# Performance work log

Hardware: AMD Instinct MI355X
Metric: run time of the kernel (lower is better)

## Reference

```python
import jax, jax.numpy as jnp
import numpy as np

SAMPLING_RATIO = 1.0


def gcn_conv(x, src, dst, ew, W, b):
    """PyG GCNConv: h = D^-1/2 (A+I) D^-1/2 (xW) + b, edges weighted by ew.
    Masked edges (ew=0) contribute neither messages nor degree, exactly
    matching running the conv on the subset edge_index."""
    n = x.shape[0]
    h = x @ W                                              # [N, out]
    deg = jax.ops.segment_sum(ew, dst, num_segments=n) + 1.0  # +1 for self-loop
    dinv = jax.lax.rsqrt(deg)                              # deg >= 1, safe
    norm = dinv[src] * dinv[dst] * ew                      # [E]
    agg = jax.ops.segment_sum(h[src] * norm[:, None], dst, num_segments=n)
    return agg + h * (dinv * dinv)[:, None] + b            # self-loop term + bias


def setup_inputs() -> dict:
    key = jax.random.key(0)
    ks = jax.random.split(key, 8)
    N, E, F_IN, HID, OUT = 50000, 800000, 128, 128, 64
    x = jax.random.normal(ks[0], (N, F_IN), dtype=jnp.float32)
    edge_index = jax.random.randint(ks[1], (2, E), 0, N, dtype=jnp.int32)
    edge_rand = jax.random.uniform(ks[2], (E,), dtype=jnp.float32)
    s0 = 1.0 / np.sqrt(F_IN)
    s1 = 1.0 / np.sqrt(HID)
    w0 = jax.random.normal(ks[3], (F_IN, HID), dtype=jnp.float32) * s0
    b0 = jnp.zeros((HID,), dtype=jnp.float32)
    w1 = jax.random.normal(ks[4], (HID, HID), dtype=jnp.float32) * s1
    b1 = jnp.zeros((HID,), dtype=jnp.float32)
    w2 = jax.random.normal(ks[5], (HID, OUT), dtype=jnp.float32) * s1
    b2 = jnp.zeros((OUT,), dtype=jnp.float32)
    return {"x": x, "edge_index": edge_index, "edge_rand": edge_rand,
            "w0": w0, "b0": b0, "w1": w1, "b1": b1, "w2": w2, "b2": b2}


def reference(x, edge_index, edge_rand, w0, b0, w1, b1, w2, b2):
    src, dst = edge_index[0], edge_index[1]
    ones = jnp.ones(src.shape, dtype=x.dtype)
    # first pass over full graph -> tmp_z
    z = jax.nn.relu(gcn_conv(x, src, dst, ones, w0, b0))
    z = jax.nn.relu(gcn_conv(z, src, dst, ones, w1, b1))
    tmp_z = gcn_conv(z, src, dst, ones, w2, b2)
    # edge sampling: gather-dot-sigmoid-threshold (detached mask)
    edge_logit = jnp.sum(tmp_z[src] * tmp_z[dst], axis=-1)
    edge_weight = jax.nn.sigmoid(edge_logit)
    mask = jax.lax.stop_gradient(
        (edge_weight > SAMPLING_RATIO * edge_rand).astype(x.dtype))
    # second pass: sampled edges for hidden layers, full edges for last layer
    h = jax.nn.relu(gcn_conv(x, src, dst, mask, w0, b0))
    h = jax.nn.relu(gcn_conv(h, src, dst, mask, w1, b1))
    out = gcn_conv(h, src, dst, ones, w2, b2)
    return out
```

## Files before the change

kernel.cpp:

```cpp
#include <hip/hip_runtime.h>


typedef __attribute__((ext_vector_type(8))) short bf16x8;
typedef __attribute__((ext_vector_type(4))) float f32x4;

__device__ inline unsigned bfpair(float lo, float hi) {
    unsigned a = __float_as_uint(lo), b = __float_as_uint(hi);
    a = (a + 0x7FFFu + ((a >> 16) & 1u)) >> 16;
    b = (b + 0x7FFFu + ((b >> 16) & 1u)) & 0xFFFF0000u;
    return a | b;
}
__device__ inline unsigned short bf1(float v) {
    unsigned u = __float_as_uint(v);
    return (unsigned short)((u + 0x7FFFu + ((u >> 16) & 1u)) >> 16);
}
__device__ inline void unpack2(unsigned u, float& f0, float& f1) {
    f0 = __uint_as_float(u << 16);
    f1 = __uint_as_float(u & 0xFFFF0000u);
}

__global__ void k_scan1(const int* __restrict__ in, int* __restrict__ out,
                        int* __restrict__ bsums, int N) {
    __shared__ int tmp[256];
    int i = blockIdx.x * 256 + threadIdx.x;
    int v = (i < N) ? in[i] : 0;
    tmp[threadIdx.x] = v;
    __syncthreads();
    for (int off = 1; off < 256; off <<= 1) {
        int t = (threadIdx.x >= off) ? tmp[threadIdx.x - off] : 0;
        __syncthreads();
        tmp[threadIdx.x] += t;
        __syncthreads();
    }
    if (i < N) out[i] = tmp[threadIdx.x] - v;
    if (threadIdx.x == 255) bsums[blockIdx.x] = tmp[255];
}

__global__ void k_scan2(int* __restrict__ bsums, int nb) {
    __shared__ int tmp[256];
    int v = (threadIdx.x < nb) ? bsums[threadIdx.x] : 0;
    tmp[threadIdx.x] = v;
    __syncthreads();
    for (int off = 1; off < 256; off <<= 1) {
        int t = (threadIdx.x >= off) ? tmp[threadIdx.x - off] : 0;
        __syncthreads();
        tmp[threadIdx.x] += t;
        __syncthreads();
    }
    if (threadIdx.x < nb) bsums[threadIdx.x] = tmp[threadIdx.x] - v;
}

__global__ void k_scan3(int* __restrict__ out, const int* __restrict__ bsums, int N, int E) {
    int i = blockIdx.x * 256 + threadIdx.x;
    if (i < N) out[i] += bsums[blockIdx.x];
    if (i == 0) out[N] = E;
}

__global__ __launch_bounds__(256) void k_bcount(const int* __restrict__ dst,
                                                int* __restrict__ cnt, int E, int chunk) {
    __shared__ int h[1024];
    for (int i = threadIdx.x; i < 1024; i += 256) h[i] = 0;
    __syncthreads();
    int beg = blockIdx.x * chunk, end = min(E, beg + chunk);
    for (int e = beg + threadIdx.x; e < end; e += 256)
        atomicAdd(&h[dst[e] >> 6], 1);
    __syncthreads();
    for (int b = threadIdx.x; b < 1024; b += 256)
        cnt[b * 64 + blockIdx.x] = h[b];
}

__global__ __launch_bounds__(256) void k_bscatter(const int* __restrict__ src,
                                                  const int* __restrict__ dst,
                                                  const float* __restrict__ er,
                                                  const int* __restrict__ sbase,
                                                  int2* __restrict__ stg, int E, int chunk) {
    __shared__ int cur[1024];
    for (int i = threadIdx.x; i < 1024; i += 256) cur[i] = 0;
    __syncthreads();
    int beg = blockIdx.x * chunk, end = min(E, beg + chunk);
    for (int e = beg + threadIdx.x; e < end; e += 256) {
        int d = dst[e];
        int b = d >> 6;
        int loc = atomicAdd(&cur[b], 1);
        int pos = sbase[b * 64 + blockIdx.x] + loc;
        stg[pos] = make_int2(src[e] | ((d & 63) << 16), (int)__float_as_uint(er[e]));
    }
}

__global__ __launch_bounds__(256) void k_bindeg(const int2* __restrict__ stg,
                                                const int* __restrict__ sbase,
                                                int* __restrict__ indeg, int N) {
    __shared__ int cnt[64];
    if (threadIdx.x < 64) cnt[threadIdx.x] = 0;
    __syncthreads();
    int b = blockIdx.x;
    int beg = sbase[b * 64], end = sbase[(b + 1) * 64];
    for (int i = beg + threadIdx.x; i < end; i += 256)
        atomicAdd(&cnt[(stg[i].x >> 16) & 63], 1);
    __syncthreads();
    if (threadIdx.x < 64) {
        int node = b * 64 + threadIdx.x;
        if (node < N) indeg[node] = cnt[threadIdx.x];
    }
}

__global__ __launch_bounds__(256) void k_bfill(const int2* __restrict__ stg,
                                               const int* __restrict__ sbase,
                                               const int* __restrict__ csr_off,
                                               const float* __restrict__ dinvF,
                                               int2* __restrict__ csr_se,
                                               float* __restrict__ coefF, int N) {
    __shared__ int cur[64];
    int b = blockIdx.x;
    if (threadIdx.x < 64) {
        int node = b * 64 + threadIdx.x;
        cur[threadIdx.x] = (node < N) ? csr_off[node] : 0;
    }
    __syncthreads();
    int beg = sbase[b * 64], end = sbase[(b + 1) * 64];
    for (int i = beg + threadIdx.x; i < end; i += 256) {
        int2 se = stg[i];
        int s = se.x & 0xFFFF;
        int j = (se.x >> 16) & 63;
        int pos = atomicAdd(&cur[j], 1);
        csr_se[pos] = make_int2(s, se.y);
        coefF[pos] = dinvF[s];
    }
}

__global__ void k_dinv(const int* __restrict__ deg, float* __restrict__ dinv, int N) {
    int i = blockIdx.x * blockDim.x + threadIdx.x;
    if (i < N) dinv[i] = 1.0f / sqrtf((float)deg[i] + 1.0f);
}

__global__ void k_coef_mask(const int2* __restrict__ csr_se, const float* __restrict__ dinv,
                            const float* __restrict__ survive, float* __restrict__ coef, int E) {
    int i = blockIdx.x * blockDim.x + threadIdx.x;
    if (i < E) coef[i] = dinv[csr_se[i].x] * survive[i];
}

__global__ __launch_bounds__(128) void k_surv(const float* __restrict__ tz,
                                              const int* __restrict__ csr_off,
                                              const int2* __restrict__ csr_se,
                                              float* __restrict__ survive,
                                              int* __restrict__ degm, int N) {
    const int v = blockIdx.x;
    const int l = threadIdx.x & 15;
    const int s = threadIdx.x >> 4;
    const int e0 = csr_off[v];
    const int e1 = csr_off[v + 1];
    const float4 tv = *(const float4*)&tz[(size_t)v * 64 + l * 4];
    int cnt = 0;
    for (int i = e0 + s; i < e1; i += 8) {
        int2 se = csr_se[i];
        const float4 a = *(const float4*)&tz[(size_t)se.x * 64 + l * 4];
        float p = a.x * tv.x + a.y * tv.y + a.z * tv.z + a.w * tv.w;
        p += __shfl_xor(p, 1, 16);
        p += __shfl_xor(p, 2, 16);
        p += __shfl_xor(p, 4, 16);
        p += __shfl_xor(p, 8, 16);
        float sg = 1.0f / (1.0f + expf(-p));
        float m = (sg > __uint_as_float((unsigned)se.y)) ? 1.0f : 0.0f;
        if (l == 0) {
            survive[i] = m;
            cnt += (m != 0.0f) ? 1 : 0;
        }
    }
    __shared__ int sc[8];
    if (l == 0) sc[s] = cnt;
    __syncthreads();
    if (threadIdx.x == 0) {
        int t = 0;
#pragma unroll
        for (int k = 0; k < 8; k++) t += sc[k];
        degm[v] = t;
    }
}

__global__ void k_packw3(const float* __restrict__ W, unsigned short* __restrict__ Wp,
                         int OUTC, int total) {
    int idx = blockIdx.x * 256 + threadIdx.x;
    if (idx >= total) return;
    int l = idx & 63;
    int tk = idx >> 6;
    int kb = tk & 3;
    int ct = tk >> 2;
    size_t PL = (size_t)(OUTC / 16) * 4 * 64 * 8;
    unsigned short v0[8], v1[8], v2[8];
#pragma unroll
    for (int i = 0; i < 8; i++) {
        float wv = W[(kb * 32 + ((l >> 4) * 8) + i) * OUTC + ct * 16 + (l & 15)];
        unsigned short h0 = bf1(wv);
        float f0 = __uint_as_float((unsigned)h0 << 16);
        float r1 = wv - f0;
        unsigned short h1 = bf1(r1);
        float f1 = __uint_as_float((unsigned)h1 << 16);
        unsigned short h2 = bf1(r1 - f1);
        v0[i] = h0; v1[i] = h1; v2[i] = h2;
    }
    auto st = [](unsigned short* dst, unsigned short* v) {
        uint4 u;
        u.x = v[0] | ((unsigned)v[1] << 16);
        u.y = v[2] | ((unsigned)v[3] << 16);
        u.z = v[4] | ((unsigned)v[5] << 16);
        u.w = v[6] | ((unsigned)v[7] << 16);
        *(uint4*)dst = u;
    };
    st(&Wp[(size_t)idx * 8], v0);
    st(&Wp[PL + (size_t)idx * 8], v1);
    st(&Wp[2 * PL + (size_t)idx * 8], v2);
}

template <int OUTC, bool WB16>
__global__ __launch_bounds__(256) void k_gemm_split(const float* __restrict__ A,
                                                    const unsigned short* __restrict__ Wp,
                                                    float* __restrict__ Cout,
                                                    unsigned short* __restrict__ Cb, int N) {
    constexpr int CT = OUTC / 16;
    constexpr int PL = CT * 4 * 64 * 8;
    constexpr int LDW = OUTC + 4;
    __shared__ float eps[64 * LDW];
    const int w = threadIdx.x >> 6;
    const int l = threadIdx.x & 63;
    int row = blockIdx.x * 64 + w * 16 + (l & 15);
    int rowc = (row < N) ? row : (N - 1);

    bf16x8 a0[4], a1[4], a2[4];
#pragma unroll
    for (int kb = 0; kb < 4; kb++) {
        const float* pa = &A[(size_t)rowc * 128 + kb * 32 + ((l >> 4) * 8)];
        float4 x0 = *(const float4*)pa;
        float4 x1 = *(const float4*)(pa + 4);
        float xa[8] = {x0.x, x0.y, x0.z, x0.w, x1.x, x1.y, x1.z, x1.w};
#pragma unroll
        for (int i = 0; i < 8; i++) {
            unsigned short h0 = bf1(xa[i]);
            float f0 = __uint_as_float((unsigned)h0 << 16);
            float r1 = xa[i] - f0;
            unsigned short h1 = bf1(r1);
            float f1 = __uint_as_float((unsigned)h1 << 16);
            unsigned short h2 = bf1(r1 - f1);
            a0[kb][i] = (short)h0;
            a1[kb][i] = (short)h1;
            a2[kb][i] = (short)h2;
        }
    }
#pragma unroll
    for (int ct = 0; ct < CT; ct++) {
        f32x4 accA = {0.f, 0.f, 0.f, 0.f};
        f32x4 accB = {0.f, 0.f, 0.f, 0.f};
#pragma unroll
        for (int kb = 0; kb < 4; kb++) {
            const size_t bo = ((size_t)(ct * 4 + kb) * 64 + l) * 8;
            bf16x8 b0 = *(const bf16x8*)&Wp[bo];
            bf16x8 b1 = *(const bf16x8*)&Wp[PL + bo];
            bf16x8 b2 = *(const bf16x8*)&Wp[2 * PL + bo];
            accA = __builtin_amdgcn_mfma_f32_16x16x32_bf16(a0[kb], b0, accA, 0, 0, 0);
            accB = __builtin_amdgcn_mfma_f32_16x16x32_bf16(a0[kb], b1, accB, 0, 0, 0);
            accA = __builtin_amdgcn_mfma_f32_16x16x32_bf16(a1[kb], b0, accA, 0, 0, 0);
            accB = __builtin_amdgcn_mfma_f32_16x16x32_bf16(a0[kb], b2, accB, 0, 0, 0);
            accA = __builtin_amdgcn_mfma_f32_16x16x32_bf16(a1[kb], b1, accA, 0, 0, 0);
            accB = __builtin_amdgcn_mfma_f32_16x16x32_bf16(a2[kb], b0, accB, 0, 0, 0);
            accA = __builtin_amdgcn_mfma_f32_16x16x32_bf16(a1[kb], b2, accA, 0, 0, 0);
            accB = __builtin_amdgcn_mfma_f32_16x16x32_bf16(a2[kb], b1, accB, 0, 0, 0);
        }
#pragma unroll
        for (int r = 0; r < 4; r++) {
            int rr = w * 16 + (l >> 4) * 4 + r;
            eps[rr * LDW + ct * 16 + (l & 15)] = accA[r] + accB[r];
        }
    }
    __syncthreads();
    constexpr int NF4 = 64 * OUTC / 4;
    for (int idx = threadIdx.x; idx < NF4; idx += 256) {
        int rl = idx / (OUTC / 4);
        int cg = idx % (OUTC / 4);
        int grow = blockIdx.x * 64 + rl;
        if (grow < N) {
            const float* sp = &eps[rl * LDW + cg * 4];
            float4 vv = make_float4(sp[0], sp[1], sp[2], sp[3]);
            *(float4*)&Cout[(size_t)grow * OUTC + cg * 4] = vv;
            if (WB16)
                *(uint2*)&Cb[(size_t)grow * OUTC + cg * 4] =
                    make_uint2(bfpair(vv.x, vv.y), bfpair(vv.z, vv.w));
        }
    }
}

template <int OUTC>
__global__ __launch_bounds__(256) void k_gemm_mfma(const unsigned short* __restrict__ A,
                                                   const unsigned short* __restrict__ Wpk,
                                                   unsigned short* __restrict__ C, int N) {
    constexpr int CT = OUTC / 16;
    __shared__ unsigned short eps[64 * OUTC];
    const int w = threadIdx.x >> 6;
    const int l = threadIdx.x & 63;
    const int rowl = (w * 16) + (l & 15);
    int row = blockIdx.x * 64 + rowl;
    int rowc = (row < N) ? row : (N - 1);

    bf16x8 a[4];
#pragma unroll
    for (int kb = 0; kb < 4; kb++)
        a[kb] = *(const bf16x8*)&A[(size_t)rowc * 128 + kb * 32 + ((l >> 4) * 8)];

#pragma unroll
    for (int ct = 0; ct < CT; ct++) {
        f32x4 acc = {0.f, 0.f, 0.f, 0.f};
#pragma unroll
        for (int kb = 0; kb < 4; kb++) {
            bf16x8 b = *(const bf16x8*)&Wpk[((size_t)(ct * 4 + kb) * 64 + l) * 8];
            acc = __builtin_amdgcn_mfma_f32_16x16x32_bf16(a[kb], b, acc, 0, 0, 0);
        }
#pragma unroll
        for (int r = 0; r < 4; r++) {
            int rr = w * 16 + (l >> 4) * 4 + r;
            eps[rr * OUTC + ct * 16 + (l & 15)] = bf1(acc[r]);
        }
    }
    __syncthreads();
    constexpr int NU4 = 64 * OUTC / 8;
    for (int idx = threadIdx.x; idx < NU4; idx += 256) {
        int rl = idx / (OUTC / 8);
        int cg = idx % (OUTC / 8);
        int grow = blockIdx.x * 64 + rl;
        if (grow < N)
            *(uint4*)&C[(size_t)grow * OUTC + cg * 8] = *(const uint4*)&eps[rl * OUTC + cg * 8];
    }
}

template <bool RELU>
__global__ __launch_bounds__(128) void k_agg128(const float* __restrict__ h,
                                                const int* __restrict__ csr_off,
                                                const int2* __restrict__ csr_se,
                                                const float* __restrict__ coef,
                                                const float* __restrict__ dinv,
                                                const float* __restrict__ bias,
                                                float* __restrict__ out, int N) {
    const int v = blockIdx.x;
    const int l = threadIdx.x & 31;
    const int s = threadIdx.x >> 5;
    const int e0 = csr_off[v];
    const int e1 = csr_off[v + 1];
    float4 acc = make_float4(0.f, 0.f, 0.f, 0.f);
    int i = e0 + s;
    for (; i + 4 < e1; i += 8) {
        int sa = csr_se[i].x;      float wa = coef[i];
        int sb = csr_se[i + 4].x;  float wb = coef[i + 4];
        float4 a = *(const float4*)&h[(size_t)sa * 128 + l * 4];
        float4 b = *(const float4*)&h[(size_t)sb * 128 + l * 4];
        acc.x = fmaf(a.x, wa, acc.x); acc.y = fmaf(a.y, wa, acc.y);
        acc.z = fmaf(a.z, wa, acc.z); acc.w = fmaf(a.w, wa, acc.w);
        acc.x = fmaf(b.x, wb, acc.x); acc.y = fmaf(b.y, wb, acc.y);
        acc.z = fmaf(b.z, wb, acc.z); acc.w = fmaf(b.w, wb, acc.w);
    }
    if (i < e1) {
        int sa = csr_se[i].x;
        float wa = coef[i];
        float4 a = *(const float4*)&h[(size_t)sa * 128 + l * 4];
        acc.x = fmaf(a.x, wa, acc.x); acc.y = fmaf(a.y, wa, acc.y);
        acc.z = fmaf(a.z, wa, acc.z); acc.w = fmaf(a.w, wa, acc.w);
    }
    __shared__ float4 red[4][32];
    red[s][l] = acc;
    __syncthreads();
    if (threadIdx.x < 32) {
        float4 r0 = red[0][l], r1 = red[1][l], r2 = red[2][l], r3 = red[3][l];
        float dv = dinv[v];
        float4 hv = *(const float4*)&h[(size_t)v * 128 + l * 4];
        float4 bb = *(const float4*)&bias[l * 4];
        float4 o;
        o.x = dv * ((r0.x + r1.x + r2.x + r3.x) + hv.x * dv) + bb.x;
        o.y = dv * ((r0.y + r1.y + r2.y + r3.y) + hv.y * dv) + bb.y;
        o.z = dv * ((r0.z + r1.z + r2.z + r3.z) + hv.z * dv) + bb.z;
        o.w = dv * ((r0.w + r1.w + r2.w + r3.w) + hv.w * dv) + bb.w;
        if (RELU) {
            o.x = fmaxf(o.x, 0.f); o.y = fmaxf(o.y, 0.f);
            o.z = fmaxf(o.z, 0.f); o.w = fmaxf(o.w, 0.f);
        }
        *(float4*)&out[(size_t)v * 128 + l * 4] = o;
    }
}

__global__ __launch_bounds__(128) void k_agg64(const float* __restrict__ h,
                                               const int* __restrict__ csr_off,
                                               const int2* __restrict__ csr_se,
                                               const float* __restrict__ coef,
                                               const float* __restrict__ dinv,
                                               const float* __restrict__ bias,
                                               float* __restrict__ out, int N) {
    const int v = blockIdx.x;
    const int l = threadIdx.x & 15;
    const int s = threadIdx.x >> 4;
    const int e0 = csr_off[v];
    const int e1 = csr_off[v + 1];
    float4 acc = make_float4(0.f, 0.f, 0.f, 0.f);
    int i = e0 + s;
    for (; i + 8 < e1; i += 16) {
        int sa = csr_se[i].x;      float wa = coef[i];
        int sb = csr_se[i + 8].x;  float wb = coef[i + 8];
        float4 a = *(const float4*)&h[(size_t)sa * 64 + l * 4];
        float4 b = *(const float4*)&h[(size_t)sb * 64 + l * 4];
        acc.x = fmaf(a.x, wa, acc.x); acc.y = fmaf(a.y, wa, acc.y);
        acc.z = fmaf(a.z, wa, acc.z); acc.w = fmaf(a.w, wa, acc.w);
        acc.x = fmaf(b.x, wb, acc.x); acc.y = fmaf(b.y, wb, acc.y);
        acc.z = fmaf(b.z, wb, acc.z); acc.w = fmaf(b.w, wb, acc.w);
    }
    if (i < e1) {
        int sa = csr_se[i].x;
        float wa = coef[i];
        float4 a = *(const float4*)&h[(size_t)sa * 64 + l * 4];
        acc.x = fmaf(a.x, wa, acc.x); acc.y = fmaf(a.y, wa, acc.y);
        acc.z = fmaf(a.z, wa, acc.z); acc.w = fmaf(a.w, wa, acc.w);
    }
    __shared__ float4 red[8][16];
    red[s][l] = acc;
    __syncthreads();
    if (threadIdx.x < 16) {
        float4 aa = make_float4(0.f, 0.f, 0.f, 0.f);
#pragma unroll
        for (int k = 0; k < 8; ++k) {
            float4 r = red[k][l];
            aa.x += r.x; aa.y += r.y; aa.z += r.z; aa.w += r.w;
        }
        float dv = dinv[v];
        float4 hv = *(const float4*)&h[(size_t)v * 64 + l * 4];
        float4 bb = *(const float4*)&bias[l * 4];
        float4 o;
        o.x = dv * (aa.x + hv.x * dv) + bb.x;
        o.y = dv * (aa.y + hv.y * dv) + bb.y;
        o.z = dv * (aa.z + hv.z * dv) + bb.z;
        o.w = dv * (aa.w + hv.w * dv) + bb.w;
        *(float4*)&out[(size_t)v * 64 + l * 4] = o;
    }
}

template <bool RELU>
__global__ __launch_bounds__(128) void k_agg128b(const unsigned short* __restrict__ h,
                                                 const int* __restrict__ csr_off,
                                                 const int2* __restrict__ csr_se,
                                                 const float* __restrict__ coef,
                                                 const float* __restrict__ dinv,
                                                 const float* __restrict__ bias,
                                                 unsigned short* __restrict__ out, int N) {
    const int v = blockIdx.x;
    const int l = threadIdx.x & 15;
    const int s = threadIdx.x >> 4;
    const int e0 = csr_off[v];
    const int e1 = csr_off[v + 1];
    float acc[8];
#pragma unroll
    for (int j = 0; j < 8; j++) acc[j] = 0.f;
    int i = e0 + s;
    for (; i + 8 < e1; i += 16) {
        int sa = csr_se[i].x;      float wa = coef[i];
        int sb = csr_se[i + 8].x;  float wb = coef[i + 8];
        uint4 ua = *(const uint4*)&h[(size_t)sa * 128 + l * 8];
        uint4 ub = *(const uint4*)&h[(size_t)sb * 128 + l * 8];
        float f0, f1;
        unpack2(ua.x, f0, f1); acc[0] = fmaf(f0, wa, acc[0]); acc[1] = fmaf(f1, wa, acc[1]);
        unpack2(ua.y, f0, f1); acc[2] = fmaf(f0, wa, acc[2]); acc[3] = fmaf(f1, wa, acc[3]);
        unpack2(ua.z, f0, f1); acc[4] = fmaf(f0, wa, acc[4]); acc[5] = fmaf(f1, wa, acc[5]);
        unpack2(ua.w, f0, f1); acc[6] = fmaf(f0, wa, acc[6]); acc[7] = fmaf(f1, wa, acc[7]);
        unpack2(ub.x, f0, f1); acc[0] = fmaf(f0, wb, acc[0]); acc[1] = fmaf(f1, wb, acc[1]);
        unpack2(ub.y, f0, f1); acc[2] = fmaf(f0, wb, acc[2]); acc[3] = fmaf(f1, wb, acc[3]);
        unpack2(ub.z, f0, f1); acc[4] = fmaf(f0, wb, acc[4]); acc[5] = fmaf(f1, wb, acc[5]);
        unpack2(ub.w, f0, f1); acc[6] = fmaf(f0, wb, acc[6]); acc[7] = fmaf(f1, wb, acc[7]);
    }
    if (i < e1) {
        int sa = csr_se[i].x;
        float wa = coef[i];
        uint4 ua = *(const uint4*)&h[(size_t)sa * 128 + l * 8];
        float f0, f1;
        unpack2(ua.x, f0, f1); acc[0] = fmaf(f0, wa, acc[0]); acc[1] = fmaf(f1, wa, acc[1]);
        unpack2(ua.y, f0, f1); acc[2] = fmaf(f0, wa, acc[2]); acc[3] = fmaf(f1, wa, acc[3]);
        unpack2(ua.z, f0, f1); acc[4] = fmaf(f0, wa, acc[4]); acc[5] = fmaf(f1, wa, acc[5]);
        unpack2(ua.w, f0, f1); acc[6] = fmaf(f0, wa, acc[6]); acc[7] = fmaf(f1, wa, acc[7]);
    }
    __shared__ float red[8][16][8];
#pragma unroll
    for (int j = 0; j < 8; j += 4)
        *(float4*)&red[s][l][j] = make_float4(acc[j], acc[j + 1], acc[j + 2], acc[j + 3]);
    __syncthreads();
    if (threadIdx.x < 16) {
        int ll = threadIdx.x;
        float rr[8];
#pragma unroll
        for (int j = 0; j < 8; j++) rr[j] = 0.f;
#pragma unroll
        for (int k = 0; k < 8; ++k)
#pragma unroll
            for (int j = 0; j < 8; j++) rr[j] += red[k][ll][j];
        float dv = dinv[v];
        uint4 uh = *(const uint4*)&h[(size_t)v * 128 + ll * 8];
        float hv[8];
        unpack2(uh.x, hv[0], hv[1]); unpack2(uh.y, hv[2], hv[3]);
        unpack2(uh.z, hv[4], hv[5]); unpack2(uh.w, hv[6], hv[7]);
        unsigned u[4];
#pragma unroll
        for (int j2 = 0; j2 < 4; j2++) {
            float o0 = dv * (rr[2 * j2 + 0] + hv[2 * j2 + 0] * dv) + bias[ll * 8 + 2 * j2 + 0];
            float o1 = dv * (rr[2 * j2 + 1] + hv[2 * j2 + 1] * dv) + bias[ll * 8 + 2 * j2 + 1];
            if (RELU) { o0 = fmaxf(o0, 0.f); o1 = fmaxf(o1, 0.f); }
            u[j2] = bfpair(o0, o1);
        }
        *(uint4*)&out[(size_t)v * 128 + ll * 8] = make_uint4(u[0], u[1], u[2], u[3]);
    }
}

__global__ __launch_bounds__(128) void k_agg64b(const unsigned short* __restrict__ h,
                                                const int* __restrict__ csr_off,
                                                const int2* __restrict__ csr_se,
                                                const float* __restrict__ coef,
                                                const float* __restrict__ dinv,
                                                const float* __restrict__ bias,
                                                float* __restrict__ out, int N) {
    const int v = blockIdx.x;
    const int l = threadIdx.x & 7;
    const int s = threadIdx.x >> 3;
    const int e0 = csr_off[v];
    const int e1 = csr_off[v + 1];
    float acc[8];
#pragma unroll
    for (int j = 0; j < 8; j++) acc[j] = 0.f;
    for (int i = e0 + s; i < e1; i += 16) {
        int sa = csr_se[i].x;
        float wa = coef[i];
        uint4 ua = *(const uint4*)&h[(size_t)sa * 64 + l * 8];
        float f0, f1;
        unpack2(ua.x, f0, f1); acc[0] = fmaf(f0, wa, acc[0]); acc[1] = fmaf(f1, wa, acc[1]);
        unpack2(ua.y, f0, f1); acc[2] = fmaf(f0, wa, acc[2]); acc[3] = fmaf(f1, wa, acc[3]);
        unpack2(ua.z, f0, f1); acc[4] = fmaf(f0, wa, acc[4]); acc[5] = fmaf(f1, wa, acc[5]);
        unpack2(ua.w, f0, f1); acc[6] = fmaf(f0, wa, acc[6]); acc[7] = fmaf(f1, wa, acc[7]);
    }
    __shared__ float red[16][8][8];
#pragma unroll
    for (int j = 0; j < 8; j += 4)
        *(float4*)&red[s][l][j] = make_float4(acc[j], acc[j + 1], acc[j + 2], acc[j + 3]);
    __syncthreads();
    if (threadIdx.x < 8) {
        int ll = threadIdx.x;
        float rr[8];
#pragma unroll
        for (int j = 0; j < 8; j++) rr[j] = 0.f;
#pragma unroll
        for (int k = 0; k < 16; ++k)
#pragma unroll
            for (int j = 0; j < 8; j++) rr[j] += red[k][ll][j];
        float dv = dinv[v];
        uint4 uh = *(const uint4*)&h[(size_t)v * 64 + ll * 8];
        float hv[8];
        unpack2(uh.x, hv[0], hv[1]); unpack2(uh.y, hv[2], hv[3]);
        unpack2(uh.z, hv[4], hv[5]); unpack2(uh.w, hv[6], hv[7]);
        float o[8];
#pragma unroll
        for (int j = 0; j < 8; j++) o[j] = dv * (rr[j] + hv[j] * dv) + bias[ll * 8 + j];
        *(float4*)&out[(size_t)v * 64 + ll * 8 + 0] = make_float4(o[0], o[1], o[2], o[3]);
        *(float4*)&out[(size_t)v * 64 + ll * 8 + 4] = make_float4(o[4], o[5], o[6], o[7]);
    }
}

extern "C" void kernel_launch(void* const* d_in, const int* in_sizes, int n_in,
                              void* d_out, int out_size, void* d_ws, size_t ws_size,
                              hipStream_t stream) {
    const float* x  = (const float*)d_in[0];
    const int*   ei = (const int*)d_in[1];
    const float* er = (const float*)d_in[2];
    const float* w0 = (const float*)d_in[3];
    const float* b0 = (const float*)d_in[4];
    const float* w1 = (const float*)d_in[5];
    const float* b1 = (const float*)d_in[6];
    const float* w2 = (const float*)d_in[7];
    const float* b2 = (const float*)d_in[8];
    const int N = in_sizes[0] / 128;
    const int E = in_sizes[2];
    const int* src  = ei;
    const int* dstv = ei + E;
    float* out = (float*)d_out;

    char* p = (char*)d_ws;
    auto alloc = [&](size_t bytes) {
        char* r = p;
        p += (bytes + 255) & ~(size_t)255;
        return r;
    };
    int* indeg     = (int*)alloc((size_t)N * 4);
    int* degm      = (int*)alloc((size_t)N * 4);
    int* csr_off   = (int*)alloc((size_t)(N + 1) * 4);
    int* bsums     = (int*)alloc(1024);
    int* bcnt      = (int*)alloc((size_t)65536 * 4);
    int* sbase     = (int*)alloc((size_t)65537 * 4);
    int2* csr_se   = (int2*)alloc((size_t)E * 8);
    int2* stg      = (int2*)alloc((size_t)E * 8);
    float* coefF   = (float*)alloc((size_t)E * 4);
    float* dinvF   = (float*)alloc((size_t)N * 4);
    float* dinvM   = (float*)alloc((size_t)N * 4);
    float* hx      = (float*)alloc((size_t)N * 128 * 4);
    unsigned short* hxb = (unsigned short*)alloc((size_t)N * 128 * 2);
    float* wk1     = (float*)alloc((size_t)N * 128 * 4);
    float* wk2     = (float*)alloc((size_t)N * 128 * 4);
    float* tz      = (float*)alloc((size_t)N * 64 * 4);
    unsigned short* w0p3 = (unsigned short*)alloc((size_t)3 * 128 * 128 * 2);
    unsigned short* w1p3 = (unsigned short*)alloc((size_t)3 * 128 * 128 * 2);
    unsigned short* w2p3 = (unsigned short*)alloc((size_t)3 * 128 * 64 * 2);
    unsigned short* wk1b = (unsigned short*)wk1;
    unsigned short* wk2b = (unsigned short*)wk2;
    float* coefM   = (float*)stg;
    float* survive = (float*)stg + E;

    const int TB = 256;
    const int ebk = (E + TB - 1) / TB;
    const int nbk = (N + TB - 1) / TB;
    const int nb = (N + 255) / 256;
    const int chunk = (E + 63) / 64;

    k_packw3<<<8, 256, 0, stream>>>(w0, w0p3, 128, 2048);
    k_packw3<<<8, 256, 0, stream>>>(w1, w1p3, 128, 2048);
    k_packw3<<<4, 256, 0, stream>>>(w2, w2p3, 64, 1024);

    k_bcount<<<64, 256, 0, stream>>>(dstv, bcnt, E, chunk);
    k_scan1<<<256, 256, 0, stream>>>(bcnt, sbase, bsums, 65536);
    k_scan2<<<1, 256, 0, stream>>>(bsums, 256);
    k_scan3<<<256, 256, 0, stream>>>(sbase, bsums, 65536, E);
    k_bscatter<<<64, 256, 0, stream>>>(src, dstv, er, sbase, stg, E, chunk);
    k_bindeg<<<1024, 256, 0, stream>>>(stg, sbase, indeg, N);
    k_scan1<<<nb, 256, 0, stream>>>(indeg, csr_off, bsums, N);
    k_scan2<<<1, 256, 0, stream>>>(bsums, nb);
    k_scan3<<<nb, 256, 0, stream>>>(csr_off, bsums, N, E);
    k_dinv<<<nbk, TB, 0, stream>>>(indeg, dinvF, N);
    k_bfill<<<1024, 256, 0, stream>>>(stg, sbase, csr_off, dinvF, csr_se, coefF, N);

    const int gbm = (N + 63) / 64;

    k_gemm_split<128, true><<<gbm, 256, 0, stream>>>(x, w0p3, hx, hxb, N);

    k_agg128<true><<<N, 128, 0, stream>>>(hx, csr_off, csr_se, coefF, dinvF, b0, wk1, N);
    k_gemm_split<128, false><<<gbm, 256, 0, stream>>>(wk1, w1p3, wk2, nullptr, N);
    k_agg128<true><<<N, 128, 0, stream>>>(wk2, csr_off, csr_se, coefF, dinvF, b1, wk1, N);
    k_gemm_split<64, false><<<gbm, 256, 0, stream>>>(wk1, w2p3, wk2, nullptr, N);
    k_agg64<<<N, 128, 0, stream>>>(wk2, csr_off, csr_se, coefF, dinvF, b2, tz, N);

    k_surv<<<N, 128, 0, stream>>>(tz, csr_off, csr_se, survive, degm, N);
    k_dinv<<<nbk, TB, 0, stream>>>(degm, dinvM, N);
    k_coef_mask<<<ebk, TB, 0, stream>>>(csr_se, dinvM, survive, coefM, E);

    k_agg128b<true><<<N, 128, 0, stream>>>(hxb, csr_off, csr_se, coefM, dinvM, b0, wk1b, N);
    k_gemm_mfma<128><<<gbm, 256, 0, stream>>>(wk1b, w1p3, wk2b, N);
    k_agg128b<true><<<N, 128, 0, stream>>>(wk2b, csr_off, csr_se, coefM, dinvM, b1, wk1b, N);
    k_gemm_mfma<64><<<gbm, 256, 0, stream>>>(wk1b, w2p3, wk2b, N);
    k_agg64b<<<N, 128, 0, stream>>>(wk2b, csr_off, csr_se, coefF, dinvF, b2, out, N);
}
```

Measured before the change: 508.0 us.

## Fold dinv and coef computations into producers; drop split-bf16 low-order products in GEMM

Computes dinvF inside the degree-binning kernel and dinvM inside the survival kernel, removing the separate dinv and coef_mask launches. The per-edge coefF/coefM arrays are eliminated, so aggregation kernels gather dinv[src] directly, and in the masked pass multiply it by survive. The three weight-packing launches merge into one. The split-precision GEMM drops the a1*b2 and a2*b1 cross terms, trading a little accuracy for fewer MFMAs. The cost is an extra random gather of dinv per edge in place of a sequential coef read.

```diff
diff --git a/kernel.cpp b/kernel.cpp
--- a/kernel.cpp
+++ b/kernel.cpp
@@ -89,7 +89,8 @@
 
 __global__ __launch_bounds__(256) void k_bindeg(const int2* __restrict__ stg,
                                                 const int* __restrict__ sbase,
-                                                int* __restrict__ indeg, int N) {
+                                                int* __restrict__ indeg,
+                                                float* __restrict__ dinvF, int N) {
     __shared__ int cnt[64];
     if (threadIdx.x < 64) cnt[threadIdx.x] = 0;
     __syncthreads();
@@ -100,16 +101,18 @@
     __syncthreads();
     if (threadIdx.x < 64) {
         int node = b * 64 + threadIdx.x;
-        if (node < N) indeg[node] = cnt[threadIdx.x];
+        if (node < N) {
+            int c = cnt[threadIdx.x];
+            indeg[node] = c;
+            dinvF[node] = 1.0f / sqrtf((float)c + 1.0f);
+        }
     }
 }
 
 __global__ __launch_bounds__(256) void k_bfill(const int2* __restrict__ stg,
                                                const int* __restrict__ sbase,
                                                const int* __restrict__ csr_off,
-                                               const float* __restrict__ dinvF,
-                                               int2* __restrict__ csr_se,
-                                               float* __restrict__ coefF, int N) {
+                                               int2* __restrict__ csr_se, int N) {
     __shared__ int cur[64];
     int b = blockIdx.x;
     if (threadIdx.x < 64) {
@@ -120,30 +123,17 @@
     int beg = sbase[b * 64], end = sbase[(b + 1) * 64];
     for (int i = beg + threadIdx.x; i < end; i += 256) {
         int2 se = stg[i];
-        int s = se.x & 0xFFFF;
         int j = (se.x >> 16) & 63;
         int pos = atomicAdd(&cur[j], 1);
-        csr_se[pos] = make_int2(s, se.y);
-        coefF[pos] = dinvF[s];
-    }
-}
-
-__global__ void k_dinv(const int* __restrict__ deg, float* __restrict__ dinv, int N) {
-    int i = blockIdx.x * blockDim.x + threadIdx.x;
-    if (i < N) dinv[i] = 1.0f / sqrtf((float)deg[i] + 1.0f);
-}
-
-__global__ void k_coef_mask(const int2* __restrict__ csr_se, const float* __restrict__ dinv,
-                            const float* __restrict__ survive, float* __restrict__ coef, int E) {
-    int i = blockIdx.x * blockDim.x + threadIdx.x;
-    if (i < E) coef[i] = dinv[csr_se[i].x] * survive[i];
+        csr_se[pos] = make_int2(se.x & 0xFFFF, se.y);
+    }
 }
 
 __global__ __launch_bounds__(128) void k_surv(const float* __restrict__ tz,
                                               const int* __restrict__ csr_off,
                                               const int2* __restrict__ csr_se,
                                               float* __restrict__ survive,
-                                              int* __restrict__ degm, int N) {
+                                              float* __restrict__ dinvM, int N) {
     const int v = blockIdx.x;
     const int l = threadIdx.x & 15;
     const int s = threadIdx.x >> 4;
@@ -173,14 +163,12 @@
         int t = 0;
 #pragma unroll
         for (int k = 0; k < 8; k++) t += sc[k];
-        degm[v] = t;
-    }
-}
-
-__global__ void k_packw3(const float* __restrict__ W, unsigned short* __restrict__ Wp,
-                         int OUTC, int total) {
-    int idx = blockIdx.x * 256 + threadIdx.x;
-    if (idx >= total) return;
+        dinvM[v] = 1.0f / sqrtf((float)t + 1.0f);
+    }
+}
+
+__device__ inline void packw3_one(const float* __restrict__ W, unsigned short* __restrict__ Wp,
+                                  int OUTC, int idx) {
     int l = idx & 63;
     int tk = idx >> 6;
     int kb = tk & 3;
@@ -209,6 +197,16 @@
     st(&Wp[(size_t)idx * 8], v0);
     st(&Wp[PL + (size_t)idx * 8], v1);
     st(&Wp[2 * PL + (size_t)idx * 8], v2);
+}
+
+__global__ void k_packw3_all(const float* __restrict__ w0, const float* __restrict__ w1,
+                             const float* __restrict__ w2,
+                             unsigned short* __restrict__ w0p, unsigned short* __restrict__ w1p,
+                             unsigned short* __restrict__ w2p) {
+    int b = blockIdx.x;
+    if (b < 8) packw3_one(w0, w0p, 128, b * 256 + threadIdx.x);
+    else if (b < 16) packw3_one(w1, w1p, 128, (b - 8) * 256 + threadIdx.x);
+    else packw3_one(w2, w2p, 64, (b - 16) * 256 + threadIdx.x);
 }
 
 template <int OUTC, bool WB16>
@@ -258,11 +256,9 @@
             accA = __builtin_amdgcn_mfma_f32_16x16x32_bf16(a0[kb], b0, accA, 0, 0, 0);
             accB = __builtin_amdgcn_mfma_f32_16x16x32_bf16(a0[kb], b1, accB, 0, 0, 0);
             accA = __builtin_amdgcn_mfma_f32_16x16x32_bf16(a1[kb], b0, accA, 0, 0, 0);
+            accB = __builtin_amdgcn_mfma_f32_16x16x32_bf16(a1[kb], b1, accB, 0, 0, 0);
+            accA = __builtin_amdgcn_mfma_f32_16x16x32_bf16(a2[kb], b0, accA, 0, 0, 0);
             accB = __builtin_amdgcn_mfma_f32_16x16x32_bf16(a0[kb], b2, accB, 0, 0, 0);
-            accA = __builtin_amdgcn_mfma_f32_16x16x32_bf16(a1[kb], b1, accA, 0, 0, 0);
-            accB = __builtin_amdgcn_mfma_f32_16x16x32_bf16(a2[kb], b0, accB, 0, 0, 0);
-            accA = __builtin_amdgcn_mfma_f32_16x16x32_bf16(a1[kb], b2, accA, 0, 0, 0);
-            accB = __builtin_amdgcn_mfma_f32_16x16x32_bf16(a2[kb], b1, accB, 0, 0, 0);
         }
 #pragma unroll
         for (int r = 0; r < 4; r++) {
@@ -333,7 +329,6 @@
 __global__ __launch_bounds__(128) void k_agg128(const float* __restrict__ h,
                                                 const int* __restrict__ csr_off,
                                                 const int2* __restrict__ csr_se,
-                                                const float* __restrict__ coef,
                                                 const float* __restrict__ dinv,
                                                 const float* __restrict__ bias,
                                                 float* __restrict__ out, int N) {
@@ -345,8 +340,8 @@
     float4 acc = make_float4(0.f, 0.f, 0.f, 0.f);
     int i = e0 + s;
     for (; i + 4 < e1; i += 8) {
-        int sa = csr_se[i].x;      float wa = coef[i];
-        int sb = csr_se[i + 4].x;  float wb = coef[i + 4];
+        int sa = csr_se[i].x;      float wa = dinv[sa];
+        int sb = csr_se[i + 4].x;  float wb = dinv[sb];
         float4 a = *(const float4*)&h[(size_t)sa * 128 + l * 4];
         float4 b = *(const float4*)&h[(size_t)sb * 128 + l * 4];
         acc.x = fmaf(a.x, wa, acc.x); acc.y = fmaf(a.y, wa, acc.y);
@@ -356,7 +351,7 @@
     }
     if (i < e1) {
         int sa = csr_se[i].x;
-        float wa = coef[i];
+        float wa = dinv[sa];
         float4 a = *(const float4*)&h[(size_t)sa * 128 + l * 4];
         acc.x = fmaf(a.x, wa, acc.x); acc.y = fmaf(a.y, wa, acc.y);
         acc.z = fmaf(a.z, wa, acc.z); acc.w = fmaf(a.w, wa, acc.w);
@@ -385,7 +380,6 @@
 __global__ __launch_bounds__(128) void k_agg64(const float* __restrict__ h,
                                                const int* __restrict__ csr_off,
                                                const int2* __restrict__ csr_se,
-                                               const float* __restrict__ coef,
                                                const float* __restrict__ dinv,
                                                const float* __restrict__ bias,
                                                float* __restrict__ out, int N) {
@@ -397,8 +391,8 @@
     float4 acc = make_float4(0.f, 0.f, 0.f, 0.f);
     int i = e0 + s;
     for (; i + 8 < e1; i += 16) {
-        int sa = csr_se[i].x;      float wa = coef[i];
-        int sb = csr_se[i + 8].x;  float wb = coef[i + 8];
+        int sa = csr_se[i].x;      float wa = dinv[sa];
+        int sb = csr_se[i + 8].x;  float wb = dinv[sb];
         float4 a = *(const float4*)&h[(size_t)sa * 64 + l * 4];
         float4 b = *(const float4*)&h[(size_t)sb * 64 + l * 4];
         acc.x = fmaf(a.x, wa, acc.x); acc.y = fmaf(a.y, wa, acc.y);
@@ -408,7 +402,7 @@
     }
     if (i < e1) {
         int sa = csr_se[i].x;
-        float wa = coef[i];
+        float wa = dinv[sa];
         float4 a = *(const float4*)&h[(size_t)sa * 64 + l * 4];
         acc.x = fmaf(a.x, wa, acc.x); acc.y = fmaf(a.y, wa, acc.y);
         acc.z = fmaf(a.z, wa, acc.z); acc.w = fmaf(a.w, wa, acc.w);
@@ -435,11 +429,11 @@
     }
 }
 
-template <bool RELU>
+template <bool RELU, bool MASKED>
 __global__ __launch_bounds__(128) void k_agg128b(const unsigned short* __restrict__ h,
                                                  const int* __restrict__ csr_off,
                                                  const int2* __restrict__ csr_se,
-                                                 const float* __restrict__ coef,
+                                                 const float* __restrict__ survive,
                                                  const float* __restrict__ dinv,
                                                  const float* __restrict__ bias,
                                                  unsigned short* __restrict__ out, int N) {
@@ -453,8 +447,10 @@
     for (int j = 0; j < 8; j++) acc[j] = 0.f;
     int i = e0 + s;
     for (; i + 8 < e1; i += 16) {
-        int sa = csr_se[i].x;      float wa = coef[i];
-        int sb = csr_se[i + 8].x;  float wb = coef[i + 8];
+        int sa = csr_se[i].x;
+        int sb = csr_se[i + 8].x;
+        float wa = MASKED ? dinv[sa] * survive[i] : dinv[sa];
+        float wb = MASKED ? dinv[sb] * survive[i + 8] : dinv[sb];
         uint4 ua = *(const uint4*)&h[(size_t)sa * 128 + l * 8];
         uint4 ub = *(const uint4*)&h[(size_t)sb * 128 + l * 8];
         float f0, f1;
@@ -469,7 +465,7 @@
     }
     if (i < e1) {
         int sa = csr_se[i].x;
-        float wa = coef[i];
+        float wa = MASKED ? dinv[sa] * survive[i] : dinv[sa];
         uint4 ua = *(const uint4*)&h[(size_t)sa * 128 + l * 8];
         float f0, f1;
         unpack2(ua.x, f0, f1); acc[0] = fmaf(f0, wa, acc[0]); acc[1] = fmaf(f1, wa, acc[1]);
@@ -511,7 +507,6 @@
 __global__ __launch_bounds__(128) void k_agg64b(const unsigned short* __restrict__ h,
                                                 const int* __restrict__ csr_off,
                                                 const int2* __restrict__ csr_se,
-                                                const float* __restrict__ coef,
                                                 const float* __restrict__ dinv,
                                                 const float* __restrict__ bias,
                                                 float* __restrict__ out, int N) {
@@ -525,7 +520,7 @@
     for (int j = 0; j < 8; j++) acc[j] = 0.f;
     for (int i = e0 + s; i < e1; i += 16) {
         int sa = csr_se[i].x;
-        float wa = coef[i];
+        float wa = dinv[sa];
         uint4 ua = *(const uint4*)&h[(size_t)sa * 64 + l * 8];
         float f0, f1;
         unpack2(ua.x, f0, f1); acc[0] = fmaf(f0, wa, acc[0]); acc[1] = fmaf(f1, wa, acc[1]);
@@ -585,14 +580,12 @@
         return r;
     };
     int* indeg     = (int*)alloc((size_t)N * 4);
-    int* degm      = (int*)alloc((size_t)N * 4);
     int* csr_off   = (int*)alloc((size_t)(N + 1) * 4);
     int* bsums     = (int*)alloc(1024);
     int* bcnt      = (int*)alloc((size_t)65536 * 4);
     int* sbase     = (int*)alloc((size_t)65537 * 4);
     int2* csr_se   = (int2*)alloc((size_t)E * 8);
     int2* stg      = (int2*)alloc((size_t)E * 8);
-    float* coefF   = (float*)alloc((size_t)E * 4);
     float* dinvF   = (float*)alloc((size_t)N * 4);
     float* dinvM   = (float*)alloc((size_t)N * 4);
     float* hx      = (float*)alloc((size_t)N * 128 * 4);
@@ -605,48 +598,39 @@
     unsigned short* w2p3 = (unsigned short*)alloc((size_t)3 * 128 * 64 * 2);
     unsigned short* wk1b = (unsigned short*)wk1;
     unsigned short* wk2b = (unsigned short*)wk2;
-    float* coefM   = (float*)stg;
-    float* survive = (float*)stg + E;
-
-    const int TB = 256;
-    const int ebk = (E + TB - 1) / TB;
-    const int nbk = (N + TB - 1) / TB;
+    float* survive = (float*)stg;
+
     const int nb = (N + 255) / 256;
     const int chunk = (E + 63) / 64;
 
-    k_packw3<<<8, 256, 0, stream>>>(w0, w0p3, 128, 2048);
-    k_packw3<<<8, 256, 0, stream>>>(w1, w1p3, 128, 2048);
-    k_packw3<<<4, 256, 0, stream>>>(w2, w2p3, 64, 1024);
+    k_packw3_all<<<20, 256, 0, stream>>>(w0, w1, w2, w0p3, w1p3, w2p3);
 
     k_bcount<<<64, 256, 0, stream>>>(dstv, bcnt, E, chunk);
     k_scan1<<<256, 256, 0, stream>>>(bcnt, sbase, bsums, 65536);
     k_scan2<<<1, 256, 0, stream>>>(bsums, 256);
     k_scan3<<<256, 256, 0, stream>>>(sbase, bsums, 65536, E);
     k_bscatter<<<64, 256, 0, stream>>>(src, dstv, er, sbase, stg, E, chunk);
-    k_bindeg<<<1024, 256, 0, stream>>>(stg, sbase, indeg, N);
+    k_bindeg<<<1024, 256, 0, stream>>>(stg, sbase, indeg, dinvF, N);
     k_scan1<<<nb, 256, 0, stream>>>(indeg, csr_off, bsums, N);
     k_scan2<<<1, 256, 0, stream>>>(bsums, nb);
     k_scan3<<<nb, 256, 0, stream>>>(csr_off, bsums, N, E);
-    k_dinv<<<nbk, TB, 0, stream>>>(indeg, dinvF, N);
-    k_bfill<<<1024, 256, 0, stream>>>(stg, sbase, csr_off, dinvF, csr_se, coefF, N);
+    k_bfill<<<1024, 256, 0, stream>>>(stg, sbase, csr_off, csr_se, N);
 
     const int gbm = (N + 63) / 64;
 
     k_gemm_split<128, true><<<gbm, 256, 0, stream>>>(x, w0p3, hx, hxb, N);
 
-    k_agg128<true><<<N, 128, 0, stream>>>(hx, csr_off, csr_se, coefF, dinvF, b0, wk1, N);
+    k_agg128<true><<<N, 128, 0, stream>>>(hx, csr_off, csr_se, dinvF, b0, wk1, N);
     k_gemm_split<128, false><<<gbm, 256, 0, stream>>>(wk1, w1p3, wk2, nullptr, N);
-    k_agg128<true><<<N, 128, 0, stream>>>(wk2, csr_off, csr_se, coefF, dinvF, b1, wk1, N);
+    k_agg128<true><<<N, 128, 0, stream>>>(wk2, csr_off, csr_se, dinvF, b1, wk1, N);
     k_gemm_split<64, false><<<gbm, 256, 0, stream>>>(wk1, w2p3, wk2, nullptr, N);
-    k_agg64<<<N, 128, 0, stream>>>(wk2, csr_off, csr_se, coefF, dinvF, b2, tz, N);
-
-    k_surv<<<N, 128, 0, stream>>>(tz, csr_off, csr_se, survive, degm, N);
-    k_dinv<<<nbk, TB, 0, stream>>>(degm, dinvM, N);
-    k_coef_mask<<<ebk, TB, 0, stream>>>(csr_se, dinvM, survive, coefM, E);
-
-    k_agg128b<true><<<N, 128, 0, stream>>>(hxb, csr_off, csr_se, coefM, dinvM, b0, wk1b, N);
+    k_agg64<<<N, 128, 0, stream>>>(wk2, csr_off, csr_se, dinvF, b2, tz, N);
+
+    k_surv<<<N, 128, 0, stream>>>(tz, csr_off, csr_se, survive, dinvM, N);
+
+    k_agg128b<true, true><<<N, 128, 0, stream>>>(hxb, csr_off, csr_se, survive, dinvM, b0, wk1b, N);
     k_gemm_mfma<128><<<gbm, 256, 0, stream>>>(wk1b, w1p3, wk2b, N);
-    k_agg128b<true><<<N, 128, 0, stream>>>(wk2b, csr_off, csr_se, coefM, dinvM, b1, wk1b, N);
+    k_agg128b<true, true><<<N, 128, 0, stream>>>(wk2b, csr_off, csr_se, survive, dinvM, b1, wk1b, N);
     k_gemm_mfma<64><<<gbm, 256, 0, stream>>>(wk1b, w2p3, wk2b, N);
-    k_agg64b<<<N, 128, 0, stream>>>(wk2b, csr_off, csr_se, coefF, dinvF, b2, out, N);
-}
+    k_agg64b<<<N, 128, 0, stream>>>(wk2b, csr_off, csr_se, dinvF, b2, out, N);
+}
```

Measured after the change: 492.0 us. -3.2%, faster.
